# Kernel tuning notes

Hardware: AMD Instinct MI355X
Metric: run time of the kernel (lower is better)

## Reference

```python
import jax, jax.numpy as jnp
import numpy as np

T, B, D, H = 2048, 8, 1024, 1024

def setup_inputs() -> dict:
    key = jax.random.key(0)
    k1, k2, k3 = jax.random.split(key, 3)
    std = 1.0 / H ** 0.5
    return {
        "x": jax.random.normal(k1, (T, B, D), dtype=jnp.float32),
        "h0": jnp.zeros((B, H), dtype=jnp.float32),
        "W_delta": jax.random.uniform(k2, (H, D), dtype=jnp.float32, minval=-0.1 * std, maxval=0.1 * std),
        "b_delta": jnp.full((H,), -1.8, dtype=jnp.float32),
        "W_B": jax.random.uniform(k3, (H, D), dtype=jnp.float32, minval=-std, maxval=std),
        "b_B": jnp.zeros((H,), dtype=jnp.float32),
    }

def reference(x, h0, W_delta, b_delta, W_B, b_B):
    # Projections over all T*B tokens at once (large GEMMs)
    delta = jax.nn.softplus(jnp.einsum('tbd,hd->tbh', x, W_delta) + b_delta)  # [T,B,H]
    decay = jnp.exp(-delta)                                                   # in (0,1)
    Bx = jnp.einsum('tbd,hd->tbh', x, W_B) + b_B                              # [T,B,H]
    # Sequential selective-decay linear recurrence: h = decay*h + (1-decay)*Bx
    def step(h, inp):
        a, bx = inp
        h_new = a * h + (1.0 - a) * bx
        return h_new, h_new
    _, hs = jax.lax.scan(step, h0, (decay, Bx))
    return hs  # [T,B,H]
```

## Files before the change

### kernel.cpp

```cpp
#include <hip/hip_runtime.h>
#include <hip/hip_bf16.h>

#define T_DIM 2048
#define B_DIM 8
#define D_DIM 1024
#define H_DIM 1024
#define M_DIM (T_DIM * B_DIM)
#define NCH (B_DIM * H_DIM)
#define CHUNK 64
#define NCHUNK (T_DIM / CHUNK)
#define NCH2 (NCH / 2)

typedef __bf16 bf16x8 __attribute__((ext_vector_type(8)));
typedef unsigned short us8 __attribute__((ext_vector_type(8)));
typedef float f32x4 __attribute__((ext_vector_type(4)));

__device__ __forceinline__ unsigned short f2bf(float f) {
    unsigned u = __float_as_uint(f);
    u += 0x7fffu + ((u >> 16) & 1u);
    return (unsigned short)(u >> 16);
}
__device__ __forceinline__ float bflo(unsigned u) { return __uint_as_float(u << 16); }
__device__ __forceinline__ float bfhi(unsigned u) { return __uint_as_float(u & 0xffff0000u); }

#define XCELLS  (M_DIM * D_DIM / 8)
#define WCELLS  (H_DIM * D_DIM / 8)
__global__ __launch_bounds__(256) void convert_kernel(
    const float* __restrict__ x, const float* __restrict__ Wd,
    const float* __restrict__ Wb, unsigned short* __restrict__ xb,
    unsigned short* __restrict__ wdb, unsigned short* __restrict__ wbb)
{
    size_t cell = (size_t)blockIdx.x * 256 + threadIdx.x;
    const float* src; unsigned short* dst;
    if (cell < XCELLS)               { src = x  + cell * 8;                    dst = xb  + cell * 8; }
    else if (cell < XCELLS + WCELLS) { size_t c = cell - XCELLS;  src = Wd + c * 8; dst = wdb + c * 8; }
    else                             { size_t c = cell - XCELLS - WCELLS; src = Wb + c * 8; dst = wbb + c * 8; }
    float4 f0 = *(const float4*)src;
    float4 f1 = *(const float4*)(src + 4);
    us8 u;
    u[0]=f2bf(f0.x); u[1]=f2bf(f0.y); u[2]=f2bf(f0.z); u[3]=f2bf(f0.w);
    u[4]=f2bf(f1.x); u[5]=f2bf(f1.y); u[6]=f2bf(f1.z); u[7]=f2bf(f1.w);
    *(us8*)dst = u;
}

__global__ __launch_bounds__(256) void proj_kernel(
    const unsigned short* __restrict__ xb, const unsigned short* __restrict__ wdb,
    const unsigned short* __restrict__ wbb, const float* __restrict__ bd,
    const float* __restrict__ bb, unsigned int* __restrict__ db)
{
    __shared__ us8 sA[1024];
    __shared__ us8 sB0[1024];
    __shared__ us8 sB1[1024];

    const int tid  = threadIdx.x;
    const int lane = tid & 63;
    const int wid  = tid >> 6;
    const int wm = wid >> 1, wn = wid & 1;
    const int bRow = blockIdx.x * 128;
    const int bCol = blockIdx.y * 128;

    f32x4 accD[4][4], accB[4][4];
    #pragma unroll
    for (int i = 0; i < 4; ++i)
        #pragma unroll
        for (int j = 0; j < 4; ++j) { accD[i][j] = (f32x4)0.0f; accB[i][j] = (f32x4)0.0f; }

    const unsigned short* aBase  = xb  + (size_t)bRow * D_DIM;
    const unsigned short* b0Base = wdb + (size_t)bCol * D_DIM;
    const unsigned short* b1Base = wbb + (size_t)bCol * D_DIM;

    for (int kt = 0; kt < D_DIM; kt += 64) {
        #pragma unroll
        for (int p = 0; p < 4; ++p) {
            int ci  = p * 256 + tid;
            int row = ci >> 3;
            int kc  = (ci & 7) ^ (row & 7);
            size_t goff = (size_t)row * D_DIM + kt + kc * 8;
            __builtin_amdgcn_global_load_lds(
                (const __attribute__((address_space(1))) unsigned int*)(aBase + goff),
                (__attribute__((address_space(3))) unsigned int*)(sA + p * 256 + wid * 64),
                16, 0, 0);
            __builtin_amdgcn_global_load_lds(
                (const __attribute__((address_space(1))) unsigned int*)(b0Base + goff),
                (__attribute__((address_space(3))) unsigned int*)(sB0 + p * 256 + wid * 64),
                16, 0, 0);
            __builtin_amdgcn_global_load_lds(
                (const __attribute__((address_space(1))) unsigned int*)(b1Base + goff),
                (__attribute__((address_space(3))) unsigned int*)(sB1 + p * 256 + wid * 64),
                16, 0, 0);
        }
        __syncthreads();

        #pragma unroll
        for (int ks = 0; ks < 2; ++ks) {
            const int kc = ks * 4 + (lane >> 4);
            bf16x8 aF[4], b0F[4], b1F[4];
            #pragma unroll
            for (int q = 0; q < 4; ++q) {
                int r = wm * 64 + q * 16 + (lane & 15);
                aF[q]  = __builtin_bit_cast(bf16x8, sA [r * 8 + (kc ^ (r & 7))]);
                int c = wn * 64 + q * 16 + (lane & 15);
                b0F[q] = __builtin_bit_cast(bf16x8, sB0[c * 8 + (kc ^ (c & 7))]);
                b1F[q] = __builtin_bit_cast(bf16x8, sB1[c * 8 + (kc ^ (c & 7))]);
            }
            #pragma unroll
            for (int nt = 0; nt < 4; ++nt)
                #pragma unroll
                for (int mt = 0; mt < 4; ++mt) {
                    accD[mt][nt] = __builtin_amdgcn_mfma_f32_16x16x32_bf16(aF[mt], b0F[nt], accD[mt][nt], 0, 0, 0);
                    accB[mt][nt] = __builtin_amdgcn_mfma_f32_16x16x32_bf16(aF[mt], b1F[nt], accB[mt][nt], 0, 0, 0);
                }
        }
        __syncthreads();
    }

    #pragma unroll
    for (int nt = 0; nt < 4; ++nt) {
        int c = bCol + wn * 64 + nt * 16 + (lane & 15);
        float bdv = bd[c], bbv = bb[c];
        #pragma unroll
        for (int mt = 0; mt < 4; ++mt) {
            int r0 = bRow + wm * 64 + mt * 16 + ((lane >> 4) << 2);
            #pragma unroll
            for (int reg = 0; reg < 4; ++reg) {
                float z  = accD[mt][nt][reg] + bdv;
                float dk = 1.0f / (1.0f + __expf(z));
                float bx = accB[mt][nt][reg] + bbv;
                db[(size_t)(r0 + reg) * H_DIM + c] =
                    (unsigned)f2bf(dk) | ((unsigned)f2bf(bx) << 16);
            }
        }
    }
}

__global__ __launch_bounds__(256) void scan_reduce(
    const uint2* __restrict__ db2, float2* __restrict__ cA, float2* __restrict__ cB)
{
    int c2 = blockIdx.y * 256 + threadIdx.x;
    int i  = blockIdx.x;
    const uint2* p = db2 + (size_t)i * CHUNK * NCH2 + c2;
    float A0 = 1.0f, B0 = 0.0f, A1 = 1.0f, B1 = 0.0f;
    for (int t = 0; t < CHUNK; ++t) {
        uint2 u = p[(size_t)t * NCH2];
        float a0 = bflo(u.x), bx0 = bfhi(u.x);
        float a1 = bflo(u.y), bx1 = bfhi(u.y);
        A0 *= a0; B0 = a0 * B0 + (1.0f - a0) * bx0;
        A1 *= a1; B1 = a1 * B1 + (1.0f - a1) * bx1;
    }
    cA[i * NCH2 + c2] = make_float2(A0, A1);
    cB[i * NCH2 + c2] = make_float2(B0, B1);
}

__global__ __launch_bounds__(256) void scan_chunks(
    const float2* __restrict__ cA, const float2* __restrict__ cB,
    const float2* __restrict__ h0, float2* __restrict__ hstart)
{
    int c2 = blockIdx.x * 256 + threadIdx.x;
    float2 h = h0[c2];
    #pragma unroll
    for (int i = 0; i < NCHUNK; ++i) {
        hstart[i * NCH2 + c2] = h;
        float2 a = cA[i * NCH2 + c2];
        float2 b = cB[i * NCH2 + c2];
        h.x = a.x * h.x + b.x;
        h.y = a.y * h.y + b.y;
    }
}

__global__ __launch_bounds__(256) void scan_apply(
    const uint2* __restrict__ db2, const float2* __restrict__ hstart,
    float2* __restrict__ out2)
{
    int c2 = blockIdx.y * 256 + threadIdx.x;
    int i  = blockIdx.x;
    float2 h = hstart[i * NCH2 + c2];
    const uint2* p = db2 + (size_t)i * CHUNK * NCH2 + c2;
    float2*      o = out2 + (size_t)i * CHUNK * NCH2 + c2;
    for (int t = 0; t < CHUNK; ++t) {
        uint2 u = p[(size_t)t * NCH2];
        float a0 = bflo(u.x), bx0 = bfhi(u.x);
        float a1 = bflo(u.y), bx1 = bfhi(u.y);
        h.x = a0 * h.x + (1.0f - a0) * bx0;
        h.y = a1 * h.y + (1.0f - a1) * bx1;
        o[(size_t)t * NCH2] = h;
    }
}

extern "C" void kernel_launch(void* const* d_in, const int* in_sizes, int n_in,
                              void* d_out, int out_size, void* d_ws, size_t ws_size,
                              hipStream_t stream) {
    const float* x  = (const float*)d_in[0];
    const float* h0 = (const float*)d_in[1];
    const float* Wd = (const float*)d_in[2];
    const float* bd = (const float*)d_in[3];
    const float* Wb = (const float*)d_in[4];
    const float* bb = (const float*)d_in[5];
    float* out = (float*)d_out;

    char* ws = (char*)d_ws;
    unsigned int* db = (unsigned int*)ws;
    float* hstart = (float*)(ws + (size_t)M_DIM * H_DIM * 4);

    char* ob = (char*)d_out;
    unsigned short* xb  = (unsigned short*)ob;
    unsigned short* wdb = (unsigned short*)(ob + ((size_t)32 << 20));
    unsigned short* wbb = (unsigned short*)(ob + ((size_t)34 << 20));
    float* cA = (float*)(ob + ((size_t)36 << 20));
    float* cB = (float*)(ob + ((size_t)37 << 20));

    convert_kernel<<<(XCELLS + 2 * WCELLS) / 256, 256, 0, stream>>>(x, Wd, Wb, xb, wdb, wbb);

    dim3 gProj(M_DIM / 128, H_DIM / 128);
    proj_kernel<<<gProj, 256, 0, stream>>>(xb, wdb, wbb, bd, bb, db);

    scan_reduce<<<dim3(NCHUNK, NCH2 / 256), 256, 0, stream>>>((const uint2*)db, (float2*)cA, (float2*)cB);
    scan_chunks<<<NCH2 / 256, 256, 0, stream>>>((const float2*)cA, (const float2*)cB, (const float2*)h0, (float2*)hstart);
    scan_apply<<<dim3(NCHUNK, NCH2 / 256), 256, 0, stream>>>((const uint2*)db, (const float2*)hstart, (float2*)out);
}
```

Measured before the change: 274.5 us.

## Double-buffer projection GEMM LDS tiles and use 8 waves per block

The projection GEMM kernel now stages the next 64-wide K tile into a second LDS buffer while computing on the current one, removing one barrier per iteration and overlapping global-to-LDS loads with MFMA work. The block grows to 512 threads in a 2x4 wave grid, so each wave holds half as many accumulators, which lowers register pressure and allows two blocks per CU. LDS use doubles to about 96KB per block, which may limit occupancy. The swizzle read index is simplified to lane&7, which relies on tile rows being aligned to 16.

```diff
diff --git a/kernel.cpp b/kernel.cpp
--- a/kernel.cpp
+++ b/kernel.cpp
@@ -43,80 +43,86 @@
     *(us8*)dst = u;
 }
 
-__global__ __launch_bounds__(256) void proj_kernel(
+__global__ __launch_bounds__(512, 2) void proj_kernel(
     const unsigned short* __restrict__ xb, const unsigned short* __restrict__ wdb,
     const unsigned short* __restrict__ wbb, const float* __restrict__ bd,
     const float* __restrict__ bb, unsigned int* __restrict__ db)
 {
-    __shared__ us8 sA[1024];
-    __shared__ us8 sB0[1024];
-    __shared__ us8 sB1[1024];
+    __shared__ us8 lds[2][3072];
 
     const int tid  = threadIdx.x;
     const int lane = tid & 63;
     const int wid  = tid >> 6;
-    const int wm = wid >> 1, wn = wid & 1;
+    const int wm = wid >> 2, wn = wid & 3;
     const int bRow = blockIdx.x * 128;
     const int bCol = blockIdx.y * 128;
 
-    f32x4 accD[4][4], accB[4][4];
+    f32x4 accD[4][2], accB[4][2];
     #pragma unroll
     for (int i = 0; i < 4; ++i)
         #pragma unroll
-        for (int j = 0; j < 4; ++j) { accD[i][j] = (f32x4)0.0f; accB[i][j] = (f32x4)0.0f; }
+        for (int j = 0; j < 2; ++j) { accD[i][j] = (f32x4)0.0f; accB[i][j] = (f32x4)0.0f; }
 
     const unsigned short* aBase  = xb  + (size_t)bRow * D_DIM;
     const unsigned short* b0Base = wdb + (size_t)bCol * D_DIM;
     const unsigned short* b1Base = wbb + (size_t)bCol * D_DIM;
 
-    for (int kt = 0; kt < D_DIM; kt += 64) {
-        #pragma unroll
-        for (int p = 0; p < 4; ++p) {
-            int ci  = p * 256 + tid;
-            int row = ci >> 3;
-            int kc  = (ci & 7) ^ (row & 7);
-            size_t goff = (size_t)row * D_DIM + kt + kc * 8;
+    auto stage = [&](int buf, int kt) {
+        #pragma unroll
+        for (int p = 0; p < 6; ++p) {
+            const unsigned short* base = (p < 2) ? aBase : (p < 4 ? b0Base : b1Base);
+            int woff = (p & 1) * 512 + wid * 64;
+            int w    = woff + lane;
+            int row  = w >> 3;
+            int kc   = (w & 7) ^ (row & 7);
             __builtin_amdgcn_global_load_lds(
-                (const __attribute__((address_space(1))) unsigned int*)(aBase + goff),
-                (__attribute__((address_space(3))) unsigned int*)(sA + p * 256 + wid * 64),
-                16, 0, 0);
-            __builtin_amdgcn_global_load_lds(
-                (const __attribute__((address_space(1))) unsigned int*)(b0Base + goff),
-                (__attribute__((address_space(3))) unsigned int*)(sB0 + p * 256 + wid * 64),
-                16, 0, 0);
-            __builtin_amdgcn_global_load_lds(
-                (const __attribute__((address_space(1))) unsigned int*)(b1Base + goff),
-                (__attribute__((address_space(3))) unsigned int*)(sB1 + p * 256 + wid * 64),
+                (const __attribute__((address_space(1))) unsigned int*)
+                    (base + (size_t)row * D_DIM + kt + kc * 8),
+                (__attribute__((address_space(3))) unsigned int*)
+                    (&lds[buf][(p >> 1) * 1024 + woff]),
                 16, 0, 0);
         }
-        __syncthreads();
-
+    };
+
+    auto compute = [&](int buf) {
         #pragma unroll
         for (int ks = 0; ks < 2; ++ks) {
             const int kc = ks * 4 + (lane >> 4);
-            bf16x8 aF[4], b0F[4], b1F[4];
-            #pragma unroll
-            for (int q = 0; q < 4; ++q) {
-                int r = wm * 64 + q * 16 + (lane & 15);
-                aF[q]  = __builtin_bit_cast(bf16x8, sA [r * 8 + (kc ^ (r & 7))]);
-                int c = wn * 64 + q * 16 + (lane & 15);
-                b0F[q] = __builtin_bit_cast(bf16x8, sB0[c * 8 + (kc ^ (c & 7))]);
-                b1F[q] = __builtin_bit_cast(bf16x8, sB1[c * 8 + (kc ^ (c & 7))]);
+            const int sl = kc ^ (lane & 7);
+            bf16x8 aF[4], b0F[2], b1F[2];
+            #pragma unroll
+            for (int mt = 0; mt < 4; ++mt) {
+                int r = wm * 64 + mt * 16 + (lane & 15);
+                aF[mt] = __builtin_bit_cast(bf16x8, lds[buf][r * 8 + sl]);
             }
             #pragma unroll
-            for (int nt = 0; nt < 4; ++nt)
+            for (int nt = 0; nt < 2; ++nt) {
+                int c = wn * 32 + nt * 16 + (lane & 15);
+                b0F[nt] = __builtin_bit_cast(bf16x8, lds[buf][1024 + c * 8 + sl]);
+                b1F[nt] = __builtin_bit_cast(bf16x8, lds[buf][2048 + c * 8 + sl]);
+            }
+            #pragma unroll
+            for (int nt = 0; nt < 2; ++nt)
                 #pragma unroll
                 for (int mt = 0; mt < 4; ++mt) {
                     accD[mt][nt] = __builtin_amdgcn_mfma_f32_16x16x32_bf16(aF[mt], b0F[nt], accD[mt][nt], 0, 0, 0);
                     accB[mt][nt] = __builtin_amdgcn_mfma_f32_16x16x32_bf16(aF[mt], b1F[nt], accB[mt][nt], 0, 0, 0);
                 }
         }
+    };
+
+    stage(0, 0);
+    __syncthreads();
+    for (int t = 0; t < 15; ++t) {
+        stage((t + 1) & 1, (t + 1) * 64);
+        compute(t & 1);
         __syncthreads();
     }
+    compute(1);
 
     #pragma unroll
-    for (int nt = 0; nt < 4; ++nt) {
-        int c = bCol + wn * 64 + nt * 16 + (lane & 15);
+    for (int nt = 0; nt < 2; ++nt) {
+        int c = bCol + wn * 32 + nt * 16 + (lane & 15);
         float bdv = bd[c], bbv = bb[c];
         #pragma unroll
         for (int mt = 0; mt < 4; ++mt) {
@@ -211,7 +217,7 @@
     convert_kernel<<<(XCELLS + 2 * WCELLS) / 256, 256, 0, stream>>>(x, Wd, Wb, xb, wdb, wbb);
 
     dim3 gProj(M_DIM / 128, H_DIM / 128);
-    proj_kernel<<<gProj, 256, 0, stream>>>(xb, wdb, wbb, bd, bb, db);
+    proj_kernel<<<gProj, 512, 0, stream>>>(xb, wdb, wbb, bd, bb, db);
 
     scan_reduce<<<dim3(NCHUNK, NCH2 / 256), 256, 0, stream>>>((const uint2*)db, (float2*)cA, (float2*)cB);
     scan_chunks<<<NCH2 / 256, 256, 0, stream>>>((const float2*)cA, (const float2*)cB, (const float2*)h0, (float2*)hstart);
```

Result: faster. 241.8 us (-11.9%).
